# Kernel tuning notes

Measured on AMD Instinct MI355X. Metric: run time of the kernel, lower is better.

The kernel has to match this reference:

```python
import jax, jax.numpy as jnp
import numpy as np

G = 8
NEIGHBORS = 9
EPS = 1e-5


def grid_sample_bilinear_border(img, grid):
    # img: [B, C, H, W], grid: [B, Hg, Wg, 2] with (x, y) in [-1, 1]
    # matches torch.nn.functional.grid_sample(mode='bilinear', padding_mode='border', align_corners=False)
    B, C, H, W = img.shape
    gx, gy = grid[..., 0], grid[..., 1]
    ix = jnp.clip(((gx + 1.0) * W - 1.0) * 0.5, 0.0, W - 1.0)
    iy = jnp.clip(((gy + 1.0) * H - 1.0) * 0.5, 0.0, H - 1.0)
    x0 = jnp.floor(ix); y0 = jnp.floor(iy)
    x1 = x0 + 1.0;      y1 = y0 + 1.0
    w00 = (x1 - ix) * (y1 - iy)
    w01 = (ix - x0) * (y1 - iy)
    w10 = (x1 - ix) * (iy - y0)
    w11 = (ix - x0) * (iy - y0)
    x0i = jnp.clip(x0, 0, W - 1).astype(jnp.int32)
    x1i = jnp.clip(x1, 0, W - 1).astype(jnp.int32)
    y0i = jnp.clip(y0, 0, H - 1).astype(jnp.int32)
    y1i = jnp.clip(y1, 0, H - 1).astype(jnp.int32)

    def gather(im, yy, xx):  # im [C,H,W], yy/xx [Hg,Wg] -> [C,Hg,Wg]
        return im[:, yy, xx]

    g = jax.vmap(gather)
    out = (g(img, y0i, x0i) * w00[:, None]
         + g(img, y0i, x1i) * w01[:, None]
         + g(img, y1i, x0i) * w10[:, None]
         + g(img, y1i, x1i) * w11[:, None])
    return out  # [B, C, Hg, Wg]


def pconv(x, w):
    # 1x1x1 conv3d (no bias): x [B,Cin,D,H,W], w [Cout,Cin]
    return jnp.einsum('bcdhw,oc->bodhw', x, w)


def bn_relu(x, gamma, beta):
    # BatchNorm3d (training-mode batch stats, biased variance) + ReLU
    mean = jnp.mean(x, axis=(0, 2, 3, 4), keepdims=True)
    var = jnp.var(x, axis=(0, 2, 3, 4), keepdims=True)
    xn = (x - mean) * jax.lax.rsqrt(var + EPS)
    return jax.nn.relu(xn * gamma.reshape(1, -1, 1, 1, 1) + beta.reshape(1, -1, 1, 1, 1))


def setup_inputs() -> dict:
    key = jax.random.key(0)
    ks = jax.random.split(key, 8)
    B, C, H, W = 2, 64, 256, 320
    ref_feature = jax.random.normal(ks[0], (B, C, H, W), dtype=jnp.float32)
    grid = jax.random.uniform(ks[1], (B, NEIGHBORS * H, W, 2), dtype=jnp.float32,
                              minval=-1.0, maxval=1.0)
    s0 = 1.0 / np.sqrt(G)
    w0 = jax.random.uniform(ks[2], (16, G), jnp.float32, -s0, s0)
    g0 = jnp.ones((16,), jnp.float32); b0 = jnp.zeros((16,), jnp.float32)
    s1 = 1.0 / np.sqrt(16)
    w1 = jax.random.uniform(ks[3], (8, 16), jnp.float32, -s1, s1)
    g1 = jnp.ones((8,), jnp.float32); b1 = jnp.zeros((8,), jnp.float32)
    s2 = 1.0 / np.sqrt(8)
    ws = jax.random.uniform(ks[4], (1, 8), jnp.float32, -s2, s2)
    bs = jax.random.uniform(ks[5], (1,), jnp.float32, -s2, s2)
    return {"ref_feature": ref_feature, "grid": grid,
            "w0": w0, "g0": g0, "b0": b0,
            "w1": w1, "g1": g1, "b1": b1,
            "ws": ws, "bs": bs}


def reference(ref_feature, grid, w0, g0, b0, w1, g1, b1, ws, bs):
    B, C, H, W = ref_feature.shape
    x = grid_sample_bilinear_border(ref_feature, grid)          # [B, C, 9H, W]
    ref = ref_feature.reshape(B, G, C // G, H, W)               # [B, G, C/G, H, W]
    x = x.reshape(B, G, C // G, NEIGHBORS, H, W)
    x = jnp.mean(x * ref[:, :, :, None], axis=2)                # [B, G, 9, H, W]
    x = bn_relu(pconv(x, w0), g0, b0)                           # [B, 16, 9, H, W]
    x = bn_relu(pconv(x, w1), g1, b1)                           # [B, 8, 9, H, W]
    s = pconv(x, ws) + bs.reshape(1, -1, 1, 1, 1)               # [B, 1, 9, H, W]
    return jax.nn.sigmoid(jnp.squeeze(s, axis=1))               # [B, 9, H, W]
```

## Files before the change

### kernel.cpp

```cpp
#include <hip/hip_runtime.h>
#include <math.h>


constexpr int   Bc  = 2;
constexpr int   Cc  = 64;
constexpr int   Hc  = 256;
constexpr int   Wc  = 320;
constexpr int   NBc = 9;
constexpr int   HWc = Hc * Wc;
constexpr int   NPIX = Bc * HWc;
constexpr int   NPT  = Bc * NBc * HWc;
constexpr float EPSV = 1e-5f;

constexpr int NBLK_S = NPIX / 32;
constexpr int NB1    = 360;
constexpr int NBT4   = NPT / 1024;

constexpr size_t OFF_FEATB = 0;
constexpr size_t OFF_SB    = OFF_FEATB + (size_t)NPIX * 32;
constexpr size_t OFF_P1    = 0;
constexpr size_t OFF_P2    = OFF_P1 + (size_t)NB1 * 64;
constexpr size_t OFF_PAR1  = OFF_P2 + (size_t)NBT4 * 16;
constexpr size_t OFF_PAR2  = OFF_PAR1 + 272;

__device__ __forceinline__ unsigned short f2bf_rne(float v) {
  unsigned int u = __float_as_uint(v);
  unsigned int r = (u + 0x7fffu + ((u >> 16) & 1u)) >> 16;
  return (unsigned short)r;
}
__device__ __forceinline__ void unpack8(uint4 u, float f[8]) {
  f[0] = __uint_as_float(u.x << 16);
  f[1] = __uint_as_float(u.x & 0xffff0000u);
  f[2] = __uint_as_float(u.y << 16);
  f[3] = __uint_as_float(u.y & 0xffff0000u);
  f[4] = __uint_as_float(u.z << 16);
  f[5] = __uint_as_float(u.z & 0xffff0000u);
  f[6] = __uint_as_float(u.w << 16);
  f[7] = __uint_as_float(u.w & 0xffff0000u);
}
__device__ __forceinline__ float dot8(const float s[8], float4 wa, float4 wb) {
  return s[0] * wa.x + s[1] * wa.y + s[2] * wa.z + s[3] * wa.w +
         s[4] * wb.x + s[5] * wb.y + s[6] * wb.z + s[7] * wb.w;
}

__global__ __launch_bounds__(256) void k_transpose(
    const float* __restrict__ feat, unsigned short* __restrict__ featB) {
  __shared__ float lds[64][65];
  const int tid  = threadIdx.x;
  const int b    = blockIdx.x / (HWc / 64);
  const int tile = blockIdx.x % (HWc / 64);
  const int hw0  = tile * 64;
  const int p    = tid & 63;
  const int ty   = tid >> 6;

  const float* src = feat + (size_t)b * Cc * HWc + hw0 + p;
#pragma unroll
  for (int c0 = 0; c0 < 64; c0 += 4) {
    lds[c0 + ty][p] = src[(size_t)(c0 + ty) * HWc];
  }
  __syncthreads();
  const int ch = tid & 63;
  unsigned short* dst = featB + ((size_t)b * HWc + hw0) * 64 + ch;
#pragma unroll
  for (int p0 = 0; p0 < 64; p0 += 4) {
    dst[(size_t)(p0 + ty) * 64] = f2bf_rne(lds[ch][p0 + ty]);
  }
}

__global__ __launch_bounds__(256) void k_sample(
    const float* __restrict__ grid, const unsigned short* __restrict__ featB,
    unsigned short* __restrict__ sOut) {
  const int tid = threadIdx.x;
  const int cid = blockIdx.x * 32 + (tid >> 3);
  const int j   = tid & 7;
  const int b   = cid / HWc;
  const int hw  = cid - b * HWc;
  const int h   = hw / Wc;
  const int w   = hw - h * Wc;

  const uint4* fbAll = (const uint4*)featB;
  const uint4 ur = fbAll[(size_t)cid * 8 + j];
  float r[8];
  unpack8(ur, r);

  const uint4* fb = fbAll + (size_t)b * HWc * 8;

#pragma unroll 3
  for (int n = 0; n < NBc; ++n) {
    const size_t gi = ((((size_t)b * NBc + n) * Hc + h) * Wc + w) * 2;
    const float2 g2 = *(const float2*)(grid + gi);
    float ix = ((g2.x + 1.f) * (float)Wc - 1.f) * 0.5f;
    float iy = ((g2.y + 1.f) * (float)Hc - 1.f) * 0.5f;
    ix = fminf(fmaxf(ix, 0.f), (float)(Wc - 1));
    iy = fminf(fmaxf(iy, 0.f), (float)(Hc - 1));
    const float x0f = floorf(ix), y0f = floorf(iy);
    const float fx = ix - x0f, fy = iy - y0f;
    const int x0 = (int)x0f, y0 = (int)y0f;
    const int x1 = min(x0 + 1, Wc - 1), y1 = min(y0 + 1, Hc - 1);
    const float w00 = (1.f - fx) * (1.f - fy);
    const float w01 = fx * (1.f - fy);
    const float w10 = (1.f - fx) * fy;
    const float w11 = fx * fy;

    const uint4 u00 = fb[(size_t)(y0 * Wc + x0) * 8 + j];
    const uint4 u01 = fb[(size_t)(y0 * Wc + x1) * 8 + j];
    const uint4 u10 = fb[(size_t)(y1 * Wc + x0) * 8 + j];
    const uint4 u11 = fb[(size_t)(y1 * Wc + x1) * 8 + j];
    float a[8], c[8], d[8], e[8];
    unpack8(u00, a);
    unpack8(u01, c);
    unpack8(u10, d);
    unpack8(u11, e);

    float s = 0.f;
#pragma unroll
    for (int k = 0; k < 8; ++k) {
      s += (w00 * a[k] + w01 * c[k] + w10 * d[k] + w11 * e[k]) * r[k];
    }
    s *= 0.125f;

    const size_t pt = ((size_t)b * NBc + n) * HWc + hw;
    sOut[pt * 8 + j] = f2bf_rne(s);
  }
}

__global__ __launch_bounds__(256) void k_stats1(
    const unsigned short* __restrict__ sB, float* __restrict__ part1) {
  float acc[44];
#pragma unroll
  for (int i = 0; i < 44; ++i) acc[i] = 0.f;
  const int tid = threadIdx.x;
  const int stride = NB1 * 256;
  for (int p = blockIdx.x * 256 + tid; p < NPT; p += stride) {
    const uint4 su = ((const uint4*)sB)[p];
    float s[8];
    unpack8(su, s);
#pragma unroll
    for (int j = 0; j < 8; ++j) acc[j] += s[j];
#pragma unroll
    for (int j = 0; j < 8; ++j) {
#pragma unroll
      for (int k = 0; k <= j; ++k) {
        acc[8 + j * (j + 1) / 2 + k] += s[j] * s[k];
      }
    }
  }
  __shared__ float red[4 * 44];
  const int wid = tid >> 6;
#pragma unroll
  for (int i = 0; i < 44; ++i) {
    float v = acc[i];
#pragma unroll
    for (int off = 32; off; off >>= 1) v += __shfl_xor(v, off);
    if ((tid & 63) == 0) red[wid * 44 + i] = v;
  }
  __syncthreads();
  if (tid < 44) {
    part1[blockIdx.x * 64 + tid] =
        red[tid] + red[44 + tid] + red[88 + tid] + red[132 + tid];
  }
}

__global__ __launch_bounds__(256) void k_reduce1(
    const float* __restrict__ part1, const float* __restrict__ w0,
    const float* __restrict__ w1, const float* __restrict__ g0,
    const float* __restrict__ b0, float* __restrict__ par1) {
  __shared__ float red[1024], totm[64], a1s[16];
  const int tid = threadIdx.x;
  {
    const int cq = tid & 15, chk = tid >> 4;
    float4 a = make_float4(0.f, 0.f, 0.f, 0.f);
    for (int r = chk; r < NB1; r += 16) {
      const float4 v = *(const float4*)(part1 + r * 64 + cq * 4);
      a.x += v.x; a.y += v.y; a.z += v.z; a.w += v.w;
    }
    red[chk * 64 + cq * 4 + 0] = a.x;
    red[chk * 64 + cq * 4 + 1] = a.y;
    red[chk * 64 + cq * 4 + 2] = a.z;
    red[chk * 64 + cq * 4 + 3] = a.w;
  }
  __syncthreads();
  if (tid < 64) {
    float v = 0.f;
#pragma unroll
    for (int k = 0; k < 16; ++k) v += red[k * 64 + tid];
    totm[tid] = v;
  }
  __syncthreads();
  if (tid < 16) {
    float wr[8];
    float mean = 0.f, ey2 = 0.f;
#pragma unroll
    for (int j = 0; j < 8; ++j) {
      wr[j] = w0[tid * 8 + j];
      mean += wr[j] * totm[j];
    }
#pragma unroll
    for (int j = 0; j < 8; ++j) {
#pragma unroll
      for (int k = 0; k <= j; ++k) {
        const float v = wr[j] * wr[k] * totm[8 + j * (j + 1) / 2 + k];
        ey2 += (k == j) ? v : 2.f * v;
      }
    }
    const float invN = 1.f / (float)NPT;
    mean *= invN;
    ey2 *= invN;
    const float var = ey2 - mean * mean;
    const float a = g0[tid] * rsqrtf(var + EPSV);
    a1s[tid] = a;
    par1[128 + tid] = b0[tid] - mean * a;
  }
  __syncthreads();
  if (tid < 128) {
    par1[tid] = a1s[tid >> 3] * w0[tid];
    par1[144 + (tid & 15) * 8 + (tid >> 4)] = w1[tid];
  }
}

__global__ __launch_bounds__(256) void k_stats2(
    const unsigned short* __restrict__ sB, const float* __restrict__ par1,
    float* __restrict__ part2) {
  __shared__ float w0ps[128], c1vs[16], w1ts[128];
  __shared__ float red[64];
  const int tid = threadIdx.x;
  if (tid < 128) {
    w0ps[tid] = par1[tid];
    w1ts[tid] = par1[144 + tid];
  }
  if (tid >= 128 && tid < 144) c1vs[tid - 128] = par1[tid];
  __syncthreads();

  const uint4* src = (const uint4*)sB + (size_t)blockIdx.x * 1024 + tid;
  float s0[8], s1[8], s2[8], s3[8];
  unpack8(src[0], s0);
  unpack8(src[256], s1);
  unpack8(src[512], s2);
  unpack8(src[768], s3);

  float z0[8], z1[8], z2[8], z3[8];
#pragma unroll
  for (int o = 0; o < 8; ++o) { z0[o] = 0.f; z1[o] = 0.f; z2[o] = 0.f; z3[o] = 0.f; }
#pragma unroll
  for (int c = 0; c < 16; ++c) {
    const float4 wa = *(const float4*)(w0ps + c * 8);
    const float4 wb = *(const float4*)(w0ps + c * 8 + 4);
    const float cc = c1vs[c];
    const float4 ta = *(const float4*)(w1ts + c * 8);
    const float4 tb = *(const float4*)(w1ts + c * 8 + 4);
    const float xa = fmaxf(dot8(s0, wa, wb) + cc, 0.f);
    const float xb = fmaxf(dot8(s1, wa, wb) + cc, 0.f);
    const float xc = fmaxf(dot8(s2, wa, wb) + cc, 0.f);
    const float xd = fmaxf(dot8(s3, wa, wb) + cc, 0.f);
    z0[0] += ta.x * xa; z0[1] += ta.y * xa; z0[2] += ta.z * xa; z0[3] += ta.w * xa;
    z0[4] += tb.x * xa; z0[5] += tb.y * xa; z0[6] += tb.z * xa; z0[7] += tb.w * xa;
    z1[0] += ta.x * xb; z1[1] += ta.y * xb; z1[2] += ta.z * xb; z1[3] += ta.w * xb;
    z1[4] += tb.x * xb; z1[5] += tb.y * xb; z1[6] += tb.z * xb; z1[7] += tb.w * xb;
    z2[0] += ta.x * xc; z2[1] += ta.y * xc; z2[2] += ta.z * xc; z2[3] += ta.w * xc;
    z2[4] += tb.x * xc; z2[5] += tb.y * xc; z2[6] += tb.z * xc; z2[7] += tb.w * xc;
    z3[0] += ta.x * xd; z3[1] += ta.y * xd; z3[2] += ta.z * xd; z3[3] += ta.w * xd;
    z3[4] += tb.x * xd; z3[5] += tb.y * xd; z3[6] += tb.z * xd; z3[7] += tb.w * xd;
  }

  const int wid = tid >> 6;
#pragma unroll
  for (int o = 0; o < 8; ++o) {
    float v = (z0[o] + z1[o]) + (z2[o] + z3[o]);
    float v2 = (z0[o] * z0[o] + z1[o] * z1[o]) + (z2[o] * z2[o] + z3[o] * z3[o]);
#pragma unroll
    for (int off = 32; off; off >>= 1) {
      v += __shfl_xor(v, off);
      v2 += __shfl_xor(v2, off);
    }
    if ((tid & 63) == 0) {
      red[wid * 16 + o] = v;
      red[wid * 16 + 8 + o] = v2;
    }
  }
  __syncthreads();
  if (tid < 16) {
    part2[blockIdx.x * 16 + tid] =
        red[tid] + red[16 + tid] + red[32 + tid] + red[48 + tid];
  }
}

__global__ __launch_bounds__(256) void k_reduce2(
    const float* __restrict__ part2, const float* __restrict__ g1,
    const float* __restrict__ b1, const float* __restrict__ wsW,
    const float* __restrict__ bs, float* __restrict__ par2) {
  __shared__ float red[1024], totz[16];
  const int tid = threadIdx.x;
  {
    const int cq = tid & 3, chk = tid >> 2;
    float4 a = make_float4(0.f, 0.f, 0.f, 0.f);
    for (int r = chk; r < NBT4; r += 64) {
      const float4 v = *(const float4*)(part2 + r * 16 + cq * 4);
      a.x += v.x; a.y += v.y; a.z += v.z; a.w += v.w;
    }
    red[chk * 16 + cq * 4 + 0] = a.x;
    red[chk * 16 + cq * 4 + 1] = a.y;
    red[chk * 16 + cq * 4 + 2] = a.z;
    red[chk * 16 + cq * 4 + 3] = a.w;
  }
  __syncthreads();
  if (tid < 16) {
    float v = 0.f;
#pragma unroll
    for (int k = 0; k < 64; ++k) v += red[k * 16 + tid];
    totz[tid] = v;
  }
  __syncthreads();
  if (tid < 8) {
    const float invN = 1.f / (float)NPT;
    const float mean = totz[tid] * invN;
    const float var = totz[8 + tid] * invN - mean * mean;
    const float a = g1[tid] * rsqrtf(var + EPSV);
    par2[tid * 4 + 0] = a;
    par2[tid * 4 + 1] = b1[tid] - mean * a;
    par2[tid * 4 + 2] = wsW[tid];
    par2[tid * 4 + 3] = 0.f;
  }
  if (tid == 8) par2[32] = bs[0];
}

__global__ __launch_bounds__(256) void k_final(
    const unsigned short* __restrict__ sB, const float* __restrict__ par1,
    const float* __restrict__ par2, float* __restrict__ out) {
  __shared__ float w0ps[128], c1vs[16], w1ts[128], w2s[33];
  const int tid = threadIdx.x;
  if (tid < 128) {
    w0ps[tid] = par1[tid];
    w1ts[tid] = par1[144 + tid];
  }
  if (tid >= 128 && tid < 144) c1vs[tid - 128] = par1[tid];
  if (tid >= 160 && tid < 193) w2s[tid - 160] = par2[tid - 160];
  __syncthreads();

  const uint4* src = (const uint4*)sB + (size_t)blockIdx.x * 1024 + tid;
  float s0[8], s1[8], s2[8], s3[8];
  unpack8(src[0], s0);
  unpack8(src[256], s1);
  unpack8(src[512], s2);
  unpack8(src[768], s3);

  float z0[8], z1[8], z2[8], z3[8];
#pragma unroll
  for (int o = 0; o < 8; ++o) { z0[o] = 0.f; z1[o] = 0.f; z2[o] = 0.f; z3[o] = 0.f; }
#pragma unroll
  for (int c = 0; c < 16; ++c) {
    const float4 wa = *(const float4*)(w0ps + c * 8);
    const float4 wb = *(const float4*)(w0ps + c * 8 + 4);
    const float cc = c1vs[c];
    const float4 ta = *(const float4*)(w1ts + c * 8);
    const float4 tb = *(const float4*)(w1ts + c * 8 + 4);
    const float xa = fmaxf(dot8(s0, wa, wb) + cc, 0.f);
    const float xb = fmaxf(dot8(s1, wa, wb) + cc, 0.f);
    const float xc = fmaxf(dot8(s2, wa, wb) + cc, 0.f);
    const float xd = fmaxf(dot8(s3, wa, wb) + cc, 0.f);
    z0[0] += ta.x * xa; z0[1] += ta.y * xa; z0[2] += ta.z * xa; z0[3] += ta.w * xa;
    z0[4] += tb.x * xa; z0[5] += tb.y * xa; z0[6] += tb.z * xa; z0[7] += tb.w * xa;
    z1[0] += ta.x * xb; z1[1] += ta.y * xb; z1[2] += ta.z * xb; z1[3] += ta.w * xb;
    z1[4] += tb.x * xb; z1[5] += tb.y * xb; z1[6] += tb.z * xb; z1[7] += tb.w * xb;
    z2[0] += ta.x * xc; z2[1] += ta.y * xc; z2[2] += ta.z * xc; z2[3] += ta.w * xc;
    z2[4] += tb.x * xc; z2[5] += tb.y * xc; z2[6] += tb.z * xc; z2[7] += tb.w * xc;
    z3[0] += ta.x * xd; z3[1] += ta.y * xd; z3[2] += ta.z * xd; z3[3] += ta.w * xd;
    z3[4] += tb.x * xd; z3[5] += tb.y * xd; z3[6] += tb.z * xd; z3[7] += tb.w * xd;
  }

  const float bsr = w2s[32];
  float r0 = bsr, r1 = bsr, r2 = bsr, r3 = bsr;
#pragma unroll
  for (int o = 0; o < 8; ++o) {
    const float4 pr = *(const float4*)(w2s + o * 4);
    r0 += pr.z * fmaxf(fmaf(pr.x, z0[o], pr.y), 0.f);
    r1 += pr.z * fmaxf(fmaf(pr.x, z1[o], pr.y), 0.f);
    r2 += pr.z * fmaxf(fmaf(pr.x, z2[o], pr.y), 0.f);
    r3 += pr.z * fmaxf(fmaf(pr.x, z3[o], pr.y), 0.f);
  }
  float* op = out + (size_t)blockIdx.x * 1024 + tid;
  op[0]   = 1.f / (1.f + __expf(-r0));
  op[256] = 1.f / (1.f + __expf(-r1));
  op[512] = 1.f / (1.f + __expf(-r2));
  op[768] = 1.f / (1.f + __expf(-r3));
}

extern "C" void kernel_launch(void* const* d_in, const int* in_sizes, int n_in,
                              void* d_out, int out_size, void* d_ws,
                              size_t ws_size, hipStream_t stream) {
  const float* feat = (const float*)d_in[0];
  const float* grid = (const float*)d_in[1];
  const float* w0 = (const float*)d_in[2];
  const float* g0 = (const float*)d_in[3];
  const float* b0 = (const float*)d_in[4];
  const float* w1 = (const float*)d_in[5];
  const float* g1 = (const float*)d_in[6];
  const float* b1 = (const float*)d_in[7];
  const float* wsW = (const float*)d_in[8];
  const float* bs = (const float*)d_in[9];
  float* out = (float*)d_out;

  float* wsf = (float*)d_ws;
  unsigned short* featB = (unsigned short*)(wsf + OFF_FEATB);
  unsigned short* sB    = (unsigned short*)(wsf + OFF_SB);
  float* part1 = wsf + OFF_P1;
  float* part2 = wsf + OFF_P2;
  float* par1  = wsf + OFF_PAR1;
  float* par2  = wsf + OFF_PAR2;

  k_transpose<<<Bc * (HWc / 64), 256, 0, stream>>>(feat, featB);
  k_sample<<<NBLK_S, 256, 0, stream>>>(grid, featB, sB);
  k_stats1<<<NB1, 256, 0, stream>>>(sB, part1);
  k_reduce1<<<1, 256, 0, stream>>>(part1, w0, w1, g0, b0, par1);
  k_stats2<<<NBT4, 256, 0, stream>>>(sB, par1, part2);
  k_reduce2<<<1, 256, 0, stream>>>(part2, g1, b1, wsW, bs, par2);
  k_final<<<NBT4, 256, 0, stream>>>(sB, par1, par2, out);
}
```

Baseline: 245.3 us.

## Fuse reduction kernels into stats kernels via last-block atomic ticket

Removes the two single-block reduce kernels by having the last block of each stats kernel, chosen by an atomic ticket counter, perform the final reduction and parameter computation. The first stats kernel switches from a grid-stride loop over 360 blocks to one block per 1024 points (NBT4 blocks), so the partials buffer is larger. Tickets live in the output buffer, are zeroed by the transpose kernel, and are later overwritten by the final kernel. This saves two kernel launches and their serialization gaps. In exchange it adds fences and atomics, and the final reduction must now sum many more partials.

```diff
diff --git a/kernel.cpp b/kernel.cpp
--- a/kernel.cpp
+++ b/kernel.cpp
@@ -13,13 +13,12 @@
 constexpr float EPSV = 1e-5f;
 
 constexpr int NBLK_S = NPIX / 32;
-constexpr int NB1    = 360;
 constexpr int NBT4   = NPT / 1024;
 
 constexpr size_t OFF_FEATB = 0;
 constexpr size_t OFF_SB    = OFF_FEATB + (size_t)NPIX * 32;
 constexpr size_t OFF_P1    = 0;
-constexpr size_t OFF_P2    = OFF_P1 + (size_t)NB1 * 64;
+constexpr size_t OFF_P2    = OFF_P1 + (size_t)NBT4 * 64;
 constexpr size_t OFF_PAR1  = OFF_P2 + (size_t)NBT4 * 16;
 constexpr size_t OFF_PAR2  = OFF_PAR1 + 272;
 
@@ -44,7 +43,9 @@
 }
 
 __global__ __launch_bounds__(256) void k_transpose(
-    const float* __restrict__ feat, unsigned short* __restrict__ featB) {
+    const float* __restrict__ feat, unsigned short* __restrict__ featB,
+    unsigned int* __restrict__ tickets) {
+  if (blockIdx.x == 0 && threadIdx.x < 2) tickets[threadIdx.x] = 0u;
   __shared__ float lds[64][65];
   const int tid  = threadIdx.x;
   const int b    = blockIdx.x / (HWc / 64);
@@ -125,16 +126,20 @@
 }
 
 __global__ __launch_bounds__(256) void k_stats1(
-    const unsigned short* __restrict__ sB, float* __restrict__ part1) {
+    const unsigned short* __restrict__ sB, const float* __restrict__ w0,
+    const float* __restrict__ g0, const float* __restrict__ b0,
+    const float* __restrict__ w1, float* __restrict__ part1,
+    float* __restrict__ par1, unsigned int* __restrict__ tickets) {
+  const int tid = threadIdx.x;
   float acc[44];
 #pragma unroll
   for (int i = 0; i < 44; ++i) acc[i] = 0.f;
-  const int tid = threadIdx.x;
-  const int stride = NB1 * 256;
-  for (int p = blockIdx.x * 256 + tid; p < NPT; p += stride) {
-    const uint4 su = ((const uint4*)sB)[p];
+
+  const uint4* src = (const uint4*)sB + (size_t)blockIdx.x * 1024 + tid;
+#pragma unroll
+  for (int i = 0; i < 4; ++i) {
     float s[8];
-    unpack8(su, s);
+    unpack8(src[i * 256], s);
 #pragma unroll
     for (int j = 0; j < 8; ++j) acc[j] += s[j];
 #pragma unroll
@@ -146,6 +151,7 @@
     }
   }
   __shared__ float red[4 * 44];
+  __shared__ int lastFlag;
   const int wid = tid >> 6;
 #pragma unroll
   for (int i = 0; i < 44; ++i) {
@@ -159,31 +165,34 @@
     part1[blockIdx.x * 64 + tid] =
         red[tid] + red[44 + tid] + red[88 + tid] + red[132 + tid];
   }
-}
-
-__global__ __launch_bounds__(256) void k_reduce1(
-    const float* __restrict__ part1, const float* __restrict__ w0,
-    const float* __restrict__ w1, const float* __restrict__ g0,
-    const float* __restrict__ b0, float* __restrict__ par1) {
-  __shared__ float red[1024], totm[64], a1s[16];
-  const int tid = threadIdx.x;
+  __threadfence();
+  __syncthreads();
+  if (tid == 0) {
+    const unsigned int old = atomicAdd(&tickets[0], 1u);
+    lastFlag = (old == (unsigned int)(NBT4 - 1));
+  }
+  __syncthreads();
+  if (!lastFlag) return;
+  __threadfence();
+
+  __shared__ float red2[1024], totm[64], a1s[16];
   {
     const int cq = tid & 15, chk = tid >> 4;
     float4 a = make_float4(0.f, 0.f, 0.f, 0.f);
-    for (int r = chk; r < NB1; r += 16) {
+    for (int r = chk; r < NBT4; r += 16) {
       const float4 v = *(const float4*)(part1 + r * 64 + cq * 4);
       a.x += v.x; a.y += v.y; a.z += v.z; a.w += v.w;
     }
-    red[chk * 64 + cq * 4 + 0] = a.x;
-    red[chk * 64 + cq * 4 + 1] = a.y;
-    red[chk * 64 + cq * 4 + 2] = a.z;
-    red[chk * 64 + cq * 4 + 3] = a.w;
+    red2[chk * 64 + cq * 4 + 0] = a.x;
+    red2[chk * 64 + cq * 4 + 1] = a.y;
+    red2[chk * 64 + cq * 4 + 2] = a.z;
+    red2[chk * 64 + cq * 4 + 3] = a.w;
   }
   __syncthreads();
   if (tid < 64) {
     float v = 0.f;
 #pragma unroll
-    for (int k = 0; k < 16; ++k) v += red[k * 64 + tid];
+    for (int k = 0; k < 16; ++k) v += red2[k * 64 + tid];
     totm[tid] = v;
   }
   __syncthreads();
@@ -220,9 +229,13 @@
 
 __global__ __launch_bounds__(256) void k_stats2(
     const unsigned short* __restrict__ sB, const float* __restrict__ par1,
-    float* __restrict__ part2) {
+    const float* __restrict__ g1, const float* __restrict__ b1,
+    const float* __restrict__ wsW, const float* __restrict__ bs,
+    float* __restrict__ part2, float* __restrict__ par2,
+    unsigned int* __restrict__ tickets) {
   __shared__ float w0ps[128], c1vs[16], w1ts[128];
   __shared__ float red[64];
+  __shared__ int lastFlag;
   const int tid = threadIdx.x;
   if (tid < 128) {
     w0ps[tid] = par1[tid];
@@ -282,14 +295,17 @@
     part2[blockIdx.x * 16 + tid] =
         red[tid] + red[16 + tid] + red[32 + tid] + red[48 + tid];
   }
-}
-
-__global__ __launch_bounds__(256) void k_reduce2(
-    const float* __restrict__ part2, const float* __restrict__ g1,
-    const float* __restrict__ b1, const float* __restrict__ wsW,
-    const float* __restrict__ bs, float* __restrict__ par2) {
-  __shared__ float red[1024], totz[16];
-  const int tid = threadIdx.x;
+  __threadfence();
+  __syncthreads();
+  if (tid == 0) {
+    const unsigned int old = atomicAdd(&tickets[1], 1u);
+    lastFlag = (old == (unsigned int)(NBT4 - 1));
+  }
+  __syncthreads();
+  if (!lastFlag) return;
+  __threadfence();
+
+  __shared__ float red2[1024], totz[16];
   {
     const int cq = tid & 3, chk = tid >> 2;
     float4 a = make_float4(0.f, 0.f, 0.f, 0.f);
@@ -297,16 +313,16 @@
       const float4 v = *(const float4*)(part2 + r * 16 + cq * 4);
       a.x += v.x; a.y += v.y; a.z += v.z; a.w += v.w;
     }
-    red[chk * 16 + cq * 4 + 0] = a.x;
-    red[chk * 16 + cq * 4 + 1] = a.y;
-    red[chk * 16 + cq * 4 + 2] = a.z;
-    red[chk * 16 + cq * 4 + 3] = a.w;
+    red2[chk * 16 + cq * 4 + 0] = a.x;
+    red2[chk * 16 + cq * 4 + 1] = a.y;
+    red2[chk * 16 + cq * 4 + 2] = a.z;
+    red2[chk * 16 + cq * 4 + 3] = a.w;
   }
   __syncthreads();
   if (tid < 16) {
     float v = 0.f;
 #pragma unroll
-    for (int k = 0; k < 64; ++k) v += red[k * 16 + tid];
+    for (int k = 0; k < 64; ++k) v += red2[k * 16 + tid];
     totz[tid] = v;
   }
   __syncthreads();
@@ -406,12 +422,12 @@
   float* part2 = wsf + OFF_P2;
   float* par1  = wsf + OFF_PAR1;
   float* par2  = wsf + OFF_PAR2;
-
-  k_transpose<<<Bc * (HWc / 64), 256, 0, stream>>>(feat, featB);
+  unsigned int* tickets = (unsigned int*)out;
+
+  k_transpose<<<Bc * (HWc / 64), 256, 0, stream>>>(feat, featB, tickets);
   k_sample<<<NBLK_S, 256, 0, stream>>>(grid, featB, sB);
-  k_stats1<<<NB1, 256, 0, stream>>>(sB, part1);
-  k_reduce1<<<1, 256, 0, stream>>>(part1, w0, w1, g0, b0, par1);
-  k_stats2<<<NBT4, 256, 0, stream>>>(sB, par1, part2);
-  k_reduce2<<<1, 256, 0, stream>>>(part2, g1, b1, wsW, bs, par2);
+  k_stats1<<<NBT4, 256, 0, stream>>>(sB, w0, g0, b0, w1, part1, par1, tickets);
+  k_stats2<<<NBT4, 256, 0, stream>>>(sB, par1, g1, b1, wsW, bs, part2, par2,
+                                     tickets);
   k_final<<<NBT4, 256, 0, stream>>>(sB, par1, par2, out);
 }
```

Result: slower. 418.3 us (+70.5%).
